# Optimization experiments

Measured on AMD Instinct MI355X. Metric: run time of the kernel, lower is better.

Reference implementation:

```python
import jax, jax.numpy as jnp
import numpy as np

B, N, C1, C2, H = 4, 4096, 320, 256, 5
HD = C1 // H  # 64


def setup_inputs() -> dict:
    key = jax.random.key(0)
    ks = jax.random.split(key, 9)
    w = lambda k, shape, fan_in: jax.random.normal(k, shape, jnp.float32) * (fan_in ** -0.5)
    return {
        "x1": jax.random.normal(ks[0], (B, N, C1), jnp.float32),
        "x2": jax.random.normal(ks[1], (B, N, C2), jnp.float32),
        # nn.Linear weights, torch layout [out_features, in_features]
        "q1_w": w(ks[2], (C1, C1), C1),
        "q2_w": w(ks[3], (C1, C2), C2),
        "kv1_w": w(ks[4], (2 * C1, C2), C2),
        "kv2_w": w(ks[5], (2 * C1, C1), C1),
        "proj1_w": w(ks[6], (C1, C1), C1),
        "proj1_b": jnp.zeros((C1,), jnp.float32),
        "proj2_w": w(ks[7], (C1, C1), C1),
        "proj2_b": jnp.zeros((C1,), jnp.float32),
    }


def _branch(xq, xkv, q_w, kv_w, proj_w, proj_b):
    b, n, _ = xq.shape
    scale = HD ** -0.5
    q = (xq @ q_w.T).reshape(b, n, H, HD).transpose(0, 2, 1, 3)          # [B,H,N,HD]
    kv = (xkv @ kv_w.T).reshape(b, n, 2, H, HD).transpose(2, 0, 3, 1, 4)  # [2,B,H,N,HD]
    k, v = kv[0], kv[1]
    attn = jax.nn.softmax(jnp.einsum('bhqd,bhkd->bhqk', q * scale, k), axis=-1)
    y = jnp.einsum('bhqk,bhkd->bhqd', attn, v)                            # [B,H,N,HD]
    y = y.transpose(0, 2, 1, 3).reshape(b, n, C1)
    return y @ proj_w.T + proj_b


def reference(x1, x2, q1_w, q2_w, kv1_w, kv2_w, proj1_w, proj1_b, proj2_w, proj2_b):
    y1 = _branch(x1, x2, q1_w, kv1_w, proj1_w, proj1_b)  # x1 queries, x2 keys/values
    y2 = _branch(x2, x1, q2_w, kv2_w, proj2_w, proj2_b)  # x2 queries, x1 keys/values
    return jnp.concatenate((y1, y2), axis=-1)            # [B,N,2*C1]
```

## Files before the change

kernel.cpp:

```cpp
#include <hip/hip_runtime.h>
#include <hip/hip_bf16.h>

#define Bb 4
#define Nn 4096
#define C1 320
#define C2 256
#define Hh 5
#define HD 64
#define Mm (Bb*Nn)

using bf16 = __hip_bfloat16;
typedef __attribute__((ext_vector_type(8))) short  short8;
typedef __attribute__((ext_vector_type(4))) short  short4_;
typedef __attribute__((ext_vector_type(4))) float  f32x4;

__device__ __forceinline__ short f2s(float f) {
    bf16 h = __float2bfloat16(f);
    short s;
    __builtin_memcpy(&s, &h, 2);
    return s;
}

__device__ __forceinline__ float fexp2(float x) {
#if __has_builtin(__builtin_amdgcn_exp2f)
    return __builtin_amdgcn_exp2f(x);
#else
    return exp2f(x);
#endif
}

__device__ __forceinline__ int swz(int row, int bb) {
    return row * 64 + ((bb ^ (row & 7)) << 3);
}

struct CvtArgs {
    const float* s[8];
    bf16* d[8];
    int off[9];
};

__global__ void cvt_all(CvtArgs a) {
    int i = (blockIdx.x * blockDim.x + threadIdx.x) * 4;
    if (i >= a.off[8]) return;
    int seg = 0;
    #pragma unroll
    for (int k = 1; k < 8; ++k) seg += (i >= a.off[k]);
    int j = i - a.off[seg];
    float4 v = *(const float4*)(a.s[seg] + j);
    short4_ o = { f2s(v.x), f2s(v.y), f2s(v.z), f2s(v.w) };
    *(short4_*)(a.d[seg] + j) = o;
}

__global__ __launch_bounds__(256) void gemm_proj(
    const bf16* __restrict__ A, const bf16* __restrict__ Wq,
    const bf16* __restrict__ Wkv, int K, float qs,
    bf16* __restrict__ Qo, bf16* __restrict__ Ko, bf16* __restrict__ Vo)
{
    __shared__ bf16 la[128 * 64];
    __shared__ bf16 lw[64 * 64];
    const int m0 = blockIdx.x * 128;
    const bool isq = blockIdx.y < 5;
    const bf16* W = isq ? Wq : Wkv;
    const int n0 = (isq ? blockIdx.y : blockIdx.y - 5) * 64;
    const int t = threadIdx.x;
    const int wave = t >> 6, lane = t & 63, l16 = lane & 15, quad = lane >> 4;
    const int sr = t >> 3, sb = t & 7;

    f32x4 acc[2][4];
    #pragma unroll
    for (int mf = 0; mf < 2; ++mf)
        #pragma unroll
        for (int nt = 0; nt < 4; ++nt) acc[mf][nt] = {0.f,0.f,0.f,0.f};

    const int nk = K >> 6;
    const bf16* ap = A + (size_t)(m0 + sr) * K + sb * 8;
    const bf16* wp = W + (size_t)(n0 + sr) * K + sb * 8;
    short8 ra0 = *(const short8*)ap;
    short8 ra1 = *(const short8*)(ap + (size_t)32 * K);
    short8 ra2 = *(const short8*)(ap + (size_t)64 * K);
    short8 ra3 = *(const short8*)(ap + (size_t)96 * K);
    short8 rw0 = *(const short8*)wp;
    short8 rw1 = *(const short8*)(wp + (size_t)32 * K);

    for (int kt = 0; kt < nk; ++kt) {
        __syncthreads();
        *(short8*)&la[swz(sr,      sb)] = ra0;
        *(short8*)&la[swz(sr + 32, sb)] = ra1;
        *(short8*)&la[swz(sr + 64, sb)] = ra2;
        *(short8*)&la[swz(sr + 96, sb)] = ra3;
        *(short8*)&lw[swz(sr,      sb)] = rw0;
        *(short8*)&lw[swz(sr + 32, sb)] = rw1;
        __syncthreads();
        if (kt + 1 < nk) {
            ap += 64; wp += 64;
            ra0 = *(const short8*)ap;
            ra1 = *(const short8*)(ap + (size_t)32 * K);
            ra2 = *(const short8*)(ap + (size_t)64 * K);
            ra3 = *(const short8*)(ap + (size_t)96 * K);
            rw0 = *(const short8*)wp;
            rw1 = *(const short8*)(wp + (size_t)32 * K);
        }
        const int arow = wave * 32 + l16;
        short8 a00 = *(const short8*)&la[swz(arow,      quad)];
        short8 a01 = *(const short8*)&la[swz(arow,      quad + 4)];
        short8 a10 = *(const short8*)&la[swz(arow + 16, quad)];
        short8 a11 = *(const short8*)&la[swz(arow + 16, quad + 4)];
        #pragma unroll
        for (int nt = 0; nt < 4; ++nt) {
            const int brow = nt * 16 + l16;
            short8 b0 = *(const short8*)&lw[swz(brow, quad)];
            short8 b1 = *(const short8*)&lw[swz(brow, quad + 4)];
            acc[0][nt] = __builtin_amdgcn_mfma_f32_16x16x32_bf16(a00, b0, acc[0][nt], 0, 0, 0);
            acc[0][nt] = __builtin_amdgcn_mfma_f32_16x16x32_bf16(a01, b1, acc[0][nt], 0, 0, 0);
            acc[1][nt] = __builtin_amdgcn_mfma_f32_16x16x32_bf16(a10, b0, acc[1][nt], 0, 0, 0);
            acc[1][nt] = __builtin_amdgcn_mfma_f32_16x16x32_bf16(a11, b1, acc[1][nt], 0, 0, 0);
        }
    }

    const bool isv = !isq && n0 >= C1;
    #pragma unroll
    for (int mf = 0; mf < 2; ++mf) {
        const int mrow = m0 + wave * 32 + mf * 16 + quad * 4;
        if (isq) {
            #pragma unroll
            for (int nt = 0; nt < 4; ++nt) {
                int col = n0 + nt * 16 + l16;
                #pragma unroll
                for (int r = 0; r < 4; ++r)
                    Qo[(size_t)(mrow + r) * C1 + col] = __float2bfloat16(acc[mf][nt][r] * qs);
            }
        } else if (!isv) {
            #pragma unroll
            for (int nt = 0; nt < 4; ++nt) {
                int col = n0 + nt * 16 + l16;
                #pragma unroll
                for (int r = 0; r < 4; ++r)
                    Ko[(size_t)(mrow + r) * C1 + col] = __float2bfloat16(acc[mf][nt][r]);
            }
        } else {
            #pragma unroll
            for (int nt = 0; nt < 4; ++nt) {
                int col = n0 + nt * 16 + l16 - C1;
                int h = col >> 6, d = col & 63;
                #pragma unroll
                for (int r = 0; r < 4; ++r) {
                    int m = mrow + r;
                    int b = m >> 12, n = m & (Nn - 1);
                    Vo[((size_t)(b * Hh + h) * 64 + d) * Nn + n] = __float2bfloat16(acc[mf][nt][r]);
                }
            }
        }
    }
}

__global__ __launch_bounds__(256) void gemm_out(
    const bf16* __restrict__ Y1, const bf16* __restrict__ Wp1, const float* __restrict__ B1,
    const bf16* __restrict__ Y2, const bf16* __restrict__ Wp2, const float* __restrict__ B2,
    float* __restrict__ Of)
{
    __shared__ bf16 la[128 * 64];
    __shared__ bf16 lw[64 * 64];
    const int zz = blockIdx.z;
    const bf16* A = zz ? Y2 : Y1;
    const bf16* W = zz ? Wp2 : Wp1;
    const float* bias = zz ? B2 : B1;
    const int ooff = zz ? C1 : 0;
    const int m0 = blockIdx.x * 128, n0 = blockIdx.y * 64;
    const int t = threadIdx.x;
    const int wave = t >> 6, lane = t & 63, l16 = lane & 15, quad = lane >> 4;
    const int sr = t >> 3, sb = t & 7;
    const int K = C1;

    f32x4 acc[2][4];
    #pragma unroll
    for (int mf = 0; mf < 2; ++mf)
        #pragma unroll
        for (int nt = 0; nt < 4; ++nt) acc[mf][nt] = {0.f,0.f,0.f,0.f};

    const int nk = K >> 6;
    const bf16* ap = A + (size_t)(m0 + sr) * K + sb * 8;
    const bf16* wp = W + (size_t)(n0 + sr) * K + sb * 8;
    short8 ra0 = *(const short8*)ap;
    short8 ra1 = *(const short8*)(ap + (size_t)32 * K);
    short8 ra2 = *(const short8*)(ap + (size_t)64 * K);
    short8 ra3 = *(const short8*)(ap + (size_t)96 * K);
    short8 rw0 = *(const short8*)wp;
    short8 rw1 = *(const short8*)(wp + (size_t)32 * K);

    for (int kt = 0; kt < nk; ++kt) {
        __syncthreads();
        *(short8*)&la[swz(sr,      sb)] = ra0;
        *(short8*)&la[swz(sr + 32, sb)] = ra1;
        *(short8*)&la[swz(sr + 64, sb)] = ra2;
        *(short8*)&la[swz(sr + 96, sb)] = ra3;
        *(short8*)&lw[swz(sr,      sb)] = rw0;
        *(short8*)&lw[swz(sr + 32, sb)] = rw1;
        __syncthreads();
        if (kt + 1 < nk) {
            ap += 64; wp += 64;
            ra0 = *(const short8*)ap;
            ra1 = *(const short8*)(ap + (size_t)32 * K);
            ra2 = *(const short8*)(ap + (size_t)64 * K);
            ra3 = *(const short8*)(ap + (size_t)96 * K);
            rw0 = *(const short8*)wp;
            rw1 = *(const short8*)(wp + (size_t)32 * K);
        }
        const int arow = wave * 32 + l16;
        short8 a00 = *(const short8*)&la[swz(arow,      quad)];
        short8 a01 = *(const short8*)&la[swz(arow,      quad + 4)];
        short8 a10 = *(const short8*)&la[swz(arow + 16, quad)];
        short8 a11 = *(const short8*)&la[swz(arow + 16, quad + 4)];
        #pragma unroll
        for (int nt = 0; nt < 4; ++nt) {
            const int brow = nt * 16 + l16;
            short8 b0 = *(const short8*)&lw[swz(brow, quad)];
            short8 b1 = *(const short8*)&lw[swz(brow, quad + 4)];
            acc[0][nt] = __builtin_amdgcn_mfma_f32_16x16x32_bf16(a00, b0, acc[0][nt], 0, 0, 0);
            acc[0][nt] = __builtin_amdgcn_mfma_f32_16x16x32_bf16(a01, b1, acc[0][nt], 0, 0, 0);
            acc[1][nt] = __builtin_amdgcn_mfma_f32_16x16x32_bf16(a10, b0, acc[1][nt], 0, 0, 0);
            acc[1][nt] = __builtin_amdgcn_mfma_f32_16x16x32_bf16(a11, b1, acc[1][nt], 0, 0, 0);
        }
    }

    #pragma unroll
    for (int mf = 0; mf < 2; ++mf) {
        const int mrow = m0 + wave * 32 + mf * 16 + quad * 4;
        #pragma unroll
        for (int nt = 0; nt < 4; ++nt) {
            int col = n0 + nt * 16 + l16;
            float bv = bias[col];
            #pragma unroll
            for (int r = 0; r < 4; ++r)
                Of[(size_t)(mrow + r) * 640 + ooff + col] = acc[mf][nt][r] + bv;
        }
    }
}

__device__ __forceinline__ unsigned cvtpk(float lo, float hi) {
    unsigned r;
    asm("v_cvt_pk_bf16_f32 %0, %1, %2" : "=v"(r) : "v"(lo), "v"(hi));
    return r;
}

__device__ __forceinline__ void plswap(unsigned &a, unsigned &b) {
#if __has_builtin(__builtin_amdgcn_permlane32_swap)
    auto r = __builtin_amdgcn_permlane32_swap(a, b, false, false);
    a = r[0]; b = r[1];
#else
    asm("v_permlane32_swap_b32 %0, %1" : "+v"(a), "+v"(b));
#endif
}

__device__ __forceinline__ short8 mk8(unsigned d0, unsigned d1, unsigned d2, unsigned d3) {
    union { unsigned u[4]; short8 s; } u;
    u.u[0] = d0; u.u[1] = d1; u.u[2] = d2; u.u[3] = d3;
    return u.s;
}

typedef __attribute__((ext_vector_type(16))) float f32x16;

__global__ __launch_bounds__(256, 2) void flash_kernel(
    const bf16* __restrict__ Q1, const bf16* __restrict__ K1,
    const bf16* __restrict__ V1, bf16* __restrict__ Y1,
    const bf16* __restrict__ Q2, const bf16* __restrict__ K2,
    const bf16* __restrict__ V2, bf16* __restrict__ Y2)
{
    __shared__ bf16 lk[64 * 64];
    __shared__ bf16 lv[64 * 64];
    const int qt = blockIdx.x, h = blockIdx.y, z = blockIdx.z;
    const int b = z & 3, branch = z >> 2;
    const bf16* Q  = branch ? Q2 : Q1;
    const bf16* Km = branch ? K2 : K1;
    const bf16* Vt = branch ? V2 : V1;
    bf16*       Yo = branch ? Y2 : Y1;

    const int t = threadIdx.x;
    const int wave = t >> 6, lane = t & 63;
    const int l32 = lane & 31, hi = lane >> 5;
    const int sr = t >> 3, sb = t & 7;

    const int qrow0 = qt * 256 + wave * 64;

    short8 qf[2][4];
    #pragma unroll
    for (int qb = 0; qb < 2; ++qb) {
        const bf16* qptr = Q + (size_t)(b * Nn + qrow0 + qb * 32 + l32) * C1 + h * HD + hi * 8;
        #pragma unroll
        for (int ksd = 0; ksd < 4; ++ksd)
            qf[qb][ksd] = *(const short8*)(qptr + ksd * 16);
    }

    f32x16 o[2][2];
    #pragma unroll
    for (int qb = 0; qb < 2; ++qb)
        #pragma unroll
        for (int db = 0; db < 2; ++db)
            o[qb][db] = (f32x16){0.f,0.f,0.f,0.f,0.f,0.f,0.f,0.f,0.f,0.f,0.f,0.f,0.f,0.f,0.f,0.f};
    float lsum[2] = {0.f, 0.f};

    const bf16* Kbase = Km + (size_t)b * Nn * C1 + h * HD;
    const bf16* Vbase = Vt + (size_t)(b * Hh + h) * 64 * Nn;

    short8 rk0 = *(const short8*)(Kbase + (size_t)sr * C1 + sb * 8);
    short8 rk1 = *(const short8*)(Kbase + (size_t)(sr + 32) * C1 + sb * 8);
    short8 rv0 = *(const short8*)(Vbase + (size_t)sr * Nn + sb * 8);
    short8 rv1 = *(const short8*)(Vbase + (size_t)(sr + 32) * Nn + sb * 8);

    const int NT = Nn / 64;
    for (int kt = 0; kt < NT; ++kt) {
        __syncthreads();
        *(short8*)&lk[swz(sr, sb)]      = rk0;
        *(short8*)&lk[swz(sr + 32, sb)] = rk1;
        *(short8*)&lv[swz(sr, sb)]      = rv0;
        *(short8*)&lv[swz(sr + 32, sb)] = rv1;
        __syncthreads();
        if (kt + 1 < NT) {
            const int kn = (kt + 1) * 64;
            rk0 = *(const short8*)(Kbase + (size_t)(kn + sr) * C1 + sb * 8);
            rk1 = *(const short8*)(Kbase + (size_t)(kn + sr + 32) * C1 + sb * 8);
            rv0 = *(const short8*)(Vbase + (size_t)sr * Nn + kn + sb * 8);
            rv1 = *(const short8*)(Vbase + (size_t)(sr + 32) * Nn + kn + sb * 8);
        }

        #pragma unroll
        for (int kb = 0; kb < 2; ++kb) {
            short8 ka[4];
            #pragma unroll
            for (int ksd = 0; ksd < 4; ++ksd)
                ka[ksd] = *(const short8*)&lk[swz(kb * 32 + l32, ksd * 2 + hi)];

            short8 pa[2][2];
            #pragma unroll
            for (int qb = 0; qb < 2; ++qb) {
                f32x16 s = (f32x16){0.f,0.f,0.f,0.f,0.f,0.f,0.f,0.f,0.f,0.f,0.f,0.f,0.f,0.f,0.f,0.f};
                #pragma unroll
                for (int ksd = 0; ksd < 4; ++ksd)
                    s = __builtin_amdgcn_mfma_f32_32x32x16_bf16(ka[ksd], qf[qb][ksd], s, 0, 0, 0);
                float p[16];
                #pragma unroll
                for (int r = 0; r < 16; ++r) p[r] = fexp2(s[r]);
                lsum[qb] += (((p[0]+p[1])+(p[2]+p[3])) + ((p[4]+p[5])+(p[6]+p[7])))
                          + (((p[8]+p[9])+(p[10]+p[11])) + ((p[12]+p[13])+(p[14]+p[15])));
                unsigned d0 = cvtpk(p[0],  p[1]),  d2 = cvtpk(p[4],  p[5]);
                plswap(d0, d2);
                unsigned d1 = cvtpk(p[2],  p[3]),  d3 = cvtpk(p[6],  p[7]);
                plswap(d1, d3);
                pa[qb][0] = mk8(d0, d1, d2, d3);
                unsigned e0 = cvtpk(p[8],  p[9]),  e2 = cvtpk(p[12], p[13]);
                plswap(e0, e2);
                unsigned e1 = cvtpk(p[10], p[11]), e3 = cvtpk(p[14], p[15]);
                plswap(e1, e3);
                pa[qb][1] = mk8(e0, e1, e2, e3);
            }

            #pragma unroll
            for (int ks = 0; ks < 2; ++ks) {
                #pragma unroll
                for (int db = 0; db < 2; ++db) {
                    short8 bv = *(const short8*)&lv[swz(db * 32 + l32, kb * 4 + ks * 2 + hi)];
                    o[0][db] = __builtin_amdgcn_mfma_f32_32x32x16_bf16(pa[0][ks], bv, o[0][db], 0, 0, 0);
                    o[1][db] = __builtin_amdgcn_mfma_f32_32x32x16_bf16(pa[1][ks], bv, o[1][db], 0, 0, 0);
                }
            }
        }
    }

    #pragma unroll
    for (int qb = 0; qb < 2; ++qb) {
        float l = lsum[qb] + __shfl_xor(lsum[qb], 32, 64);
        float inv = 1.0f / l;
        #pragma unroll
        for (int r = 0; r < 16; ++r) {
            const int qr = (r & 3) + 8 * (r >> 2) + 4 * hi;
            float invr = __shfl(inv, qr, 64);
            size_t row = (size_t)(b * Nn + qrow0 + qb * 32 + qr);
            #pragma unroll
            for (int db = 0; db < 2; ++db)
                Yo[row * C1 + h * HD + db * 32 + l32] = __float2bfloat16(o[qb][db][r] * invr);
        }
    }
}

extern "C" void kernel_launch(void* const* d_in, const int* in_sizes, int n_in,
                              void* d_out, int out_size, void* d_ws, size_t ws_size,
                              hipStream_t stream)
{
    const float* x1   = (const float*)d_in[0];
    const float* x2   = (const float*)d_in[1];
    const float* q1w  = (const float*)d_in[2];
    const float* q2w  = (const float*)d_in[3];
    const float* kv1w = (const float*)d_in[4];
    const float* kv2w = (const float*)d_in[5];
    const float* p1w  = (const float*)d_in[6];
    const float* p1b  = (const float*)d_in[7];
    const float* p2w  = (const float*)d_in[8];
    const float* p2b  = (const float*)d_in[9];
    float* out = (float*)d_out;

    bf16* ws = (bf16*)d_ws;
    size_t o = 0;
    bf16* x1b  = ws + o; o += (size_t)Mm * C1;
    bf16* x2b  = ws + o; o += (size_t)Mm * C2;
    bf16* wq1  = ws + o; o += C1 * C1;
    bf16* wq2  = ws + o; o += C1 * C2;
    bf16* wkv1 = ws + o; o += 2 * C1 * C2;
    bf16* wkv2 = ws + o; o += 2 * C1 * C1;
    bf16* wp1  = ws + o; o += C1 * C1;
    bf16* wp2  = ws + o; o += C1 * C1;
    bf16* Q1   = ws + o; o += (size_t)Mm * C1;
    bf16* K1   = ws + o; o += (size_t)Mm * C1;
    bf16* V1t  = ws + o; o += (size_t)Mm * C1;
    bf16* Q2   = ws + o; o += (size_t)Mm * C1;
    bf16* K2   = ws + o; o += (size_t)Mm * C1;
    bf16* V2t  = ws + o; o += (size_t)Mm * C1;
    bf16* Y1   = ws + o; o += (size_t)Mm * C1;
    bf16* Y2   = ws + o; o += (size_t)Mm * C1;
    (void)ws_size; (void)in_sizes; (void)n_in; (void)out_size;

    CvtArgs ca;
    ca.s[0] = x1;   ca.d[0] = x1b;  int n0 = Mm * C1;
    ca.s[1] = x2;   ca.d[1] = x2b;  int n1 = Mm * C2;
    ca.s[2] = q1w;  ca.d[2] = wq1;  int n2 = C1 * C1;
    ca.s[3] = q2w;  ca.d[3] = wq2;  int n3 = C1 * C2;
    ca.s[4] = kv1w; ca.d[4] = wkv1; int n4 = 2 * C1 * C2;
    ca.s[5] = kv2w; ca.d[5] = wkv2; int n5 = 2 * C1 * C1;
    ca.s[6] = p1w;  ca.d[6] = wp1;  int n6 = C1 * C1;
    ca.s[7] = p2w;  ca.d[7] = wp2;  int n7 = C1 * C1;
    int ns[8] = {n0, n1, n2, n3, n4, n5, n6, n7};
    ca.off[0] = 0;
    for (int i = 0; i < 8; ++i) ca.off[i + 1] = ca.off[i] + ns[i];
    int total = ca.off[8];
    cvt_all<<<dim3((total / 4 + 255) / 256), 256, 0, stream>>>(ca);

    const float QS = 0.125f * 1.4426950408889634f;

    gemm_proj<<<dim3(Mm / 128, 15), 256, 0, stream>>>(x1b, wq1, wkv2, C1, QS, Q1, K2, V2t);
    gemm_proj<<<dim3(Mm / 128, 15), 256, 0, stream>>>(x2b, wq2, wkv1, C2, QS, Q2, K1, V1t);

    flash_kernel<<<dim3(Nn / 256, Hh, 2 * Bb), 256, 0, stream>>>(Q1, K1, V1t, Y1, Q2, K2, V2t, Y2);

    gemm_out<<<dim3(Mm / 128, C1 / 64, 2), 256, 0, stream>>>(Y1, wp1, p1b, Y2, wp2, p2b, out);
}
```

Measured before the change: 351.0 us.

## Merge projection GEMMs into one launch and halve flash attention block size

The two QKV projection GEMM launches become a single launch with a doubled grid. Each block picks its input, weights, K dimension and outputs from blockIdx.y. The flash attention kernel now uses 128-thread blocks (2 waves, 128 query rows) instead of 256, with the K/V tile staging loop rewritten so each thread loads four rows. This doubles the flash grid to spread work over more CUs and removes one launch, at the cost of each K/V tile being reused by fewer query rows, which doubles K/V global and LDS traffic per query.

Measured after the change: 348.2 us. About the same (-0.8%).

```diff
diff --git a/kernel.cpp b/kernel.cpp
--- a/kernel.cpp
+++ b/kernel.cpp
@@ -13,6 +13,7 @@
 typedef __attribute__((ext_vector_type(8))) short  short8;
 typedef __attribute__((ext_vector_type(4))) short  short4_;
 typedef __attribute__((ext_vector_type(4))) float  f32x4;
+typedef __attribute__((ext_vector_type(16))) float f32x16;
 
 __device__ __forceinline__ short f2s(float f) {
     bf16 h = __float2bfloat16(f);
@@ -33,6 +34,27 @@
     return row * 64 + ((bb ^ (row & 7)) << 3);
 }
 
+__device__ __forceinline__ unsigned cvtpk(float lo, float hi) {
+    unsigned r;
+    asm("v_cvt_pk_bf16_f32 %0, %1, %2" : "=v"(r) : "v"(lo), "v"(hi));
+    return r;
+}
+
+__device__ __forceinline__ void plswap(unsigned &a, unsigned &b) {
+#if __has_builtin(__builtin_amdgcn_permlane32_swap)
+    auto r = __builtin_amdgcn_permlane32_swap(a, b, false, false);
+    a = r[0]; b = r[1];
+#else
+    asm("v_permlane32_swap_b32 %0, %1" : "+v"(a), "+v"(b));
+#endif
+}
+
+__device__ __forceinline__ short8 mk8(unsigned d0, unsigned d1, unsigned d2, unsigned d3) {
+    union { unsigned u[4]; short8 s; } u;
+    u.u[0] = d0; u.u[1] = d1; u.u[2] = d2; u.u[3] = d3;
+    return u.s;
+}
+
 struct CvtArgs {
     const float* s[8];
     bf16* d[8];
@@ -52,16 +74,26 @@
 }
 
 __global__ __launch_bounds__(256) void gemm_proj(
-    const bf16* __restrict__ A, const bf16* __restrict__ Wq,
-    const bf16* __restrict__ Wkv, int K, float qs,
-    bf16* __restrict__ Qo, bf16* __restrict__ Ko, bf16* __restrict__ Vo)
+    const bf16* __restrict__ A1, const bf16* __restrict__ Wq1, const bf16* __restrict__ Wkv1,
+    const bf16* __restrict__ A2, const bf16* __restrict__ Wq2, const bf16* __restrict__ Wkv2,
+    float qs,
+    bf16* __restrict__ Qo1, bf16* __restrict__ Ko1, bf16* __restrict__ Vo1,
+    bf16* __restrict__ Qo2, bf16* __restrict__ Ko2, bf16* __restrict__ Vo2)
 {
     __shared__ bf16 la[128 * 64];
     __shared__ bf16 lw[64 * 64];
     const int m0 = blockIdx.x * 128;
-    const bool isq = blockIdx.y < 5;
-    const bf16* W = isq ? Wq : Wkv;
-    const int n0 = (isq ? blockIdx.y : blockIdx.y - 5) * 64;
+    const int by = blockIdx.y;
+    const int g = (by >= 15);
+    const int yy = by - 15 * g;
+    const int K = g ? C2 : C1;
+    const bf16* A = g ? A2 : A1;
+    const bool isq = yy < 5;
+    const bf16* W = isq ? (g ? Wq2 : Wq1) : (g ? Wkv2 : Wkv1);
+    bf16* Qo = g ? Qo2 : Qo1;
+    bf16* Ko = g ? Ko2 : Ko1;
+    bf16* Vo = g ? Vo2 : Vo1;
+    const int n0 = (isq ? yy : yy - 5) * 64;
     const int t = threadIdx.x;
     const int wave = t >> 6, lane = t & 63, l16 = lane & 15, quad = lane >> 4;
     const int sr = t >> 3, sb = t & 7;
@@ -236,30 +268,7 @@
     }
 }
 
-__device__ __forceinline__ unsigned cvtpk(float lo, float hi) {
-    unsigned r;
-    asm("v_cvt_pk_bf16_f32 %0, %1, %2" : "=v"(r) : "v"(lo), "v"(hi));
-    return r;
-}
-
-__device__ __forceinline__ void plswap(unsigned &a, unsigned &b) {
-#if __has_builtin(__builtin_amdgcn_permlane32_swap)
-    auto r = __builtin_amdgcn_permlane32_swap(a, b, false, false);
-    a = r[0]; b = r[1];
-#else
-    asm("v_permlane32_swap_b32 %0, %1" : "+v"(a), "+v"(b));
-#endif
-}
-
-__device__ __forceinline__ short8 mk8(unsigned d0, unsigned d1, unsigned d2, unsigned d3) {
-    union { unsigned u[4]; short8 s; } u;
-    u.u[0] = d0; u.u[1] = d1; u.u[2] = d2; u.u[3] = d3;
-    return u.s;
-}
-
-typedef __attribute__((ext_vector_type(16))) float f32x16;
-
-__global__ __launch_bounds__(256, 2) void flash_kernel(
+__global__ __launch_bounds__(128, 2) void flash_kernel(
     const bf16* __restrict__ Q1, const bf16* __restrict__ K1,
     const bf16* __restrict__ V1, bf16* __restrict__ Y1,
     const bf16* __restrict__ Q2, const bf16* __restrict__ K2,
@@ -279,7 +288,7 @@
     const int l32 = lane & 31, hi = lane >> 5;
     const int sr = t >> 3, sb = t & 7;
 
-    const int qrow0 = qt * 256 + wave * 64;
+    const int qrow0 = qt * 128 + wave * 64;
 
     short8 qf[2][4];
     #pragma unroll
@@ -301,25 +310,33 @@
     const bf16* Kbase = Km + (size_t)b * Nn * C1 + h * HD;
     const bf16* Vbase = Vt + (size_t)(b * Hh + h) * 64 * Nn;
 
-    short8 rk0 = *(const short8*)(Kbase + (size_t)sr * C1 + sb * 8);
-    short8 rk1 = *(const short8*)(Kbase + (size_t)(sr + 32) * C1 + sb * 8);
-    short8 rv0 = *(const short8*)(Vbase + (size_t)sr * Nn + sb * 8);
-    short8 rv1 = *(const short8*)(Vbase + (size_t)(sr + 32) * Nn + sb * 8);
+    const bf16* kp[4];
+    const bf16* vp[4];
+    short8 rk[4], rv[4];
+    #pragma unroll
+    for (int i = 0; i < 4; ++i) {
+        kp[i] = Kbase + (size_t)(sr + 16 * i) * C1 + sb * 8;
+        vp[i] = Vbase + (size_t)(sr + 16 * i) * Nn + sb * 8;
+        rk[i] = *(const short8*)kp[i];
+        rv[i] = *(const short8*)vp[i];
+    }
 
     const int NT = Nn / 64;
     for (int kt = 0; kt < NT; ++kt) {
         __syncthreads();
-        *(short8*)&lk[swz(sr, sb)]      = rk0;
-        *(short8*)&lk[swz(sr + 32, sb)] = rk1;
-        *(short8*)&lv[swz(sr, sb)]      = rv0;
-        *(short8*)&lv[swz(sr + 32, sb)] = rv1;
+        #pragma unroll
+        for (int i = 0; i < 4; ++i) {
+            *(short8*)&lk[swz(sr + 16 * i, sb)] = rk[i];
+            *(short8*)&lv[swz(sr + 16 * i, sb)] = rv[i];
+        }
         __syncthreads();
         if (kt + 1 < NT) {
-            const int kn = (kt + 1) * 64;
-            rk0 = *(const short8*)(Kbase + (size_t)(kn + sr) * C1 + sb * 8);
-            rk1 = *(const short8*)(Kbase + (size_t)(kn + sr + 32) * C1 + sb * 8);
-            rv0 = *(const short8*)(Vbase + (size_t)sr * Nn + kn + sb * 8);
-            rv1 = *(const short8*)(Vbase + (size_t)(sr + 32) * Nn + kn + sb * 8);
+            #pragma unroll
+            for (int i = 0; i < 4; ++i) {
+                kp[i] += 64 * C1; vp[i] += 64;
+                rk[i] = *(const short8*)kp[i];
+                rv[i] = *(const short8*)vp[i];
+            }
         }
 
         #pragma unroll
@@ -434,10 +451,11 @@
 
     const float QS = 0.125f * 1.4426950408889634f;
 
-    gemm_proj<<<dim3(Mm / 128, 15), 256, 0, stream>>>(x1b, wq1, wkv2, C1, QS, Q1, K2, V2t);
-    gemm_proj<<<dim3(Mm / 128, 15), 256, 0, stream>>>(x2b, wq2, wkv1, C2, QS, Q2, K1, V1t);
-
-    flash_kernel<<<dim3(Nn / 256, Hh, 2 * Bb), 256, 0, stream>>>(Q1, K1, V1t, Y1, Q2, K2, V2t, Y2);
+    gemm_proj<<<dim3(Mm / 128, 30), 256, 0, stream>>>(
+        x1b, wq1, wkv2, x2b, wq2, wkv1, QS,
+        Q1, K2, V2t, Q2, K1, V1t);
+
+    flash_kernel<<<dim3(Nn / 128, Hh, 2 * Bb), 128, 0, stream>>>(Q1, K1, V1t, Y1, Q2, K2, V2t, Y2);
 
     gemm_out<<<dim3(Mm / 128, C1 / 64, 2), 256, 0, stream>>>(Y1, wp1, p1b, Y2, wp2, p2b, out);
 }
```

## Merge projection GEMM launches and shrink flash query tile for more occupancy

Applied to the files above, without the earlier changes.

Fuses the two QKV projection GEMM launches into one grid with 30 column blocks, selecting inputs and weights per block from blockIdx.y. This saves a launch and lets both halves fill the GPU together. The flash attention kernel drops from 64 to 32 query rows per wave (128 per block), doubling the grid and raising launch bounds to 4 blocks per CU. The aim is more waves to hide latency, at the cost of loading K/V tiles twice as often per query row, which halves K/V reuse.

Result: slower. 364.6 us (+3.9%).

```diff
diff --git a/kernel.cpp b/kernel.cpp
--- a/kernel.cpp
+++ b/kernel.cpp
@@ -13,6 +13,7 @@
 typedef __attribute__((ext_vector_type(8))) short  short8;
 typedef __attribute__((ext_vector_type(4))) short  short4_;
 typedef __attribute__((ext_vector_type(4))) float  f32x4;
+typedef __attribute__((ext_vector_type(16))) float f32x16;
 
 __device__ __forceinline__ short f2s(float f) {
     bf16 h = __float2bfloat16(f);
@@ -31,6 +32,27 @@
 
 __device__ __forceinline__ int swz(int row, int bb) {
     return row * 64 + ((bb ^ (row & 7)) << 3);
+}
+
+__device__ __forceinline__ unsigned cvtpk(float lo, float hi) {
+    unsigned r;
+    asm("v_cvt_pk_bf16_f32 %0, %1, %2" : "=v"(r) : "v"(lo), "v"(hi));
+    return r;
+}
+
+__device__ __forceinline__ void plswap(unsigned &a, unsigned &b) {
+#if __has_builtin(__builtin_amdgcn_permlane32_swap)
+    auto r = __builtin_amdgcn_permlane32_swap(a, b, false, false);
+    a = r[0]; b = r[1];
+#else
+    asm("v_permlane32_swap_b32 %0, %1" : "+v"(a), "+v"(b));
+#endif
+}
+
+__device__ __forceinline__ short8 mk8(unsigned d0, unsigned d1, unsigned d2, unsigned d3) {
+    union { unsigned u[4]; short8 s; } u;
+    u.u[0] = d0; u.u[1] = d1; u.u[2] = d2; u.u[3] = d3;
+    return u.s;
 }
 
 struct CvtArgs {
@@ -52,16 +74,26 @@
 }
 
 __global__ __launch_bounds__(256) void gemm_proj(
-    const bf16* __restrict__ A, const bf16* __restrict__ Wq,
-    const bf16* __restrict__ Wkv, int K, float qs,
-    bf16* __restrict__ Qo, bf16* __restrict__ Ko, bf16* __restrict__ Vo)
+    const bf16* __restrict__ A1, const bf16* __restrict__ Wq1, const bf16* __restrict__ Wkv1,
+    const bf16* __restrict__ A2, const bf16* __restrict__ Wq2, const bf16* __restrict__ Wkv2,
+    float qs,
+    bf16* __restrict__ Qo1, bf16* __restrict__ Ko1, bf16* __restrict__ Vo1,
+    bf16* __restrict__ Qo2, bf16* __restrict__ Ko2, bf16* __restrict__ Vo2)
 {
     __shared__ bf16 la[128 * 64];
     __shared__ bf16 lw[64 * 64];
     const int m0 = blockIdx.x * 128;
-    const bool isq = blockIdx.y < 5;
-    const bf16* W = isq ? Wq : Wkv;
-    const int n0 = (isq ? blockIdx.y : blockIdx.y - 5) * 64;
+    const int by = blockIdx.y;
+    const int g = (by >= 15);
+    const int yy = by - 15 * g;
+    const int K = g ? C2 : C1;
+    const bf16* A = g ? A2 : A1;
+    const bool isq = yy < 5;
+    const bf16* W = isq ? (g ? Wq2 : Wq1) : (g ? Wkv2 : Wkv1);
+    bf16* Qo = g ? Qo2 : Qo1;
+    bf16* Ko = g ? Ko2 : Ko1;
+    bf16* Vo = g ? Vo2 : Vo1;
+    const int n0 = (isq ? yy : yy - 5) * 64;
     const int t = threadIdx.x;
     const int wave = t >> 6, lane = t & 63, l16 = lane & 15, quad = lane >> 4;
     const int sr = t >> 3, sb = t & 7;
@@ -236,30 +268,7 @@
     }
 }
 
-__device__ __forceinline__ unsigned cvtpk(float lo, float hi) {
-    unsigned r;
-    asm("v_cvt_pk_bf16_f32 %0, %1, %2" : "=v"(r) : "v"(lo), "v"(hi));
-    return r;
-}
-
-__device__ __forceinline__ void plswap(unsigned &a, unsigned &b) {
-#if __has_builtin(__builtin_amdgcn_permlane32_swap)
-    auto r = __builtin_amdgcn_permlane32_swap(a, b, false, false);
-    a = r[0]; b = r[1];
-#else
-    asm("v_permlane32_swap_b32 %0, %1" : "+v"(a), "+v"(b));
-#endif
-}
-
-__device__ __forceinline__ short8 mk8(unsigned d0, unsigned d1, unsigned d2, unsigned d3) {
-    union { unsigned u[4]; short8 s; } u;
-    u.u[0] = d0; u.u[1] = d1; u.u[2] = d2; u.u[3] = d3;
-    return u.s;
-}
-
-typedef __attribute__((ext_vector_type(16))) float f32x16;
-
-__global__ __launch_bounds__(256, 2) void flash_kernel(
+__global__ __launch_bounds__(256, 4) void flash_kernel(
     const bf16* __restrict__ Q1, const bf16* __restrict__ K1,
     const bf16* __restrict__ V1, bf16* __restrict__ Y1,
     const bf16* __restrict__ Q2, const bf16* __restrict__ K2,
@@ -279,24 +288,20 @@
     const int l32 = lane & 31, hi = lane >> 5;
     const int sr = t >> 3, sb = t & 7;
 
-    const int qrow0 = qt * 256 + wave * 64;
-
-    short8 qf[2][4];
-    #pragma unroll
-    for (int qb = 0; qb < 2; ++qb) {
-        const bf16* qptr = Q + (size_t)(b * Nn + qrow0 + qb * 32 + l32) * C1 + h * HD + hi * 8;
+    const int qrow0 = qt * 128 + wave * 32;
+
+    short8 qf[4];
+    {
+        const bf16* qptr = Q + (size_t)(b * Nn + qrow0 + l32) * C1 + h * HD + hi * 8;
         #pragma unroll
         for (int ksd = 0; ksd < 4; ++ksd)
-            qf[qb][ksd] = *(const short8*)(qptr + ksd * 16);
-    }
-
-    f32x16 o[2][2];
-    #pragma unroll
-    for (int qb = 0; qb < 2; ++qb)
-        #pragma unroll
-        for (int db = 0; db < 2; ++db)
-            o[qb][db] = (f32x16){0.f,0.f,0.f,0.f,0.f,0.f,0.f,0.f,0.f,0.f,0.f,0.f,0.f,0.f,0.f,0.f};
-    float lsum[2] = {0.f, 0.f};
+            qf[ksd] = *(const short8*)(qptr + ksd * 16);
+    }
+
+    f32x16 o[2];
+    o[0] = (f32x16){0.f,0.f,0.f,0.f,0.f,0.f,0.f,0.f,0.f,0.f,0.f,0.f,0.f,0.f,0.f,0.f};
+    o[1] = o[0];
+    float lsum = 0.f;
 
     const bf16* Kbase = Km + (size_t)b * Nn * C1 + h * HD;
     const bf16* Vbase = Vt + (size_t)(b * Hh + h) * 64 * Nn;
@@ -329,28 +334,29 @@
             for (int ksd = 0; ksd < 4; ++ksd)
                 ka[ksd] = *(const short8*)&lk[swz(kb * 32 + l32, ksd * 2 + hi)];
 
-            short8 pa[2][2];
-            #pragma unroll
-            for (int qb = 0; qb < 2; ++qb) {
-                f32x16 s = (f32x16){0.f,0.f,0.f,0.f,0.f,0.f,0.f,0.f,0.f,0.f,0.f,0.f,0.f,0.f,0.f,0.f};
-                #pragma unroll
-                for (int ksd = 0; ksd < 4; ++ksd)
-                    s = __builtin_amdgcn_mfma_f32_32x32x16_bf16(ka[ksd], qf[qb][ksd], s, 0, 0, 0);
-                float p[16];
-                #pragma unroll
-                for (int r = 0; r < 16; ++r) p[r] = fexp2(s[r]);
-                lsum[qb] += (((p[0]+p[1])+(p[2]+p[3])) + ((p[4]+p[5])+(p[6]+p[7])))
-                          + (((p[8]+p[9])+(p[10]+p[11])) + ((p[12]+p[13])+(p[14]+p[15])));
+            f32x16 s = (f32x16){0.f,0.f,0.f,0.f,0.f,0.f,0.f,0.f,0.f,0.f,0.f,0.f,0.f,0.f,0.f,0.f};
+            #pragma unroll
+            for (int ksd = 0; ksd < 4; ++ksd)
+                s = __builtin_amdgcn_mfma_f32_32x32x16_bf16(ka[ksd], qf[ksd], s, 0, 0, 0);
+
+            float p[16];
+            #pragma unroll
+            for (int r = 0; r < 16; ++r) p[r] = fexp2(s[r]);
+            lsum += (((p[0]+p[1])+(p[2]+p[3])) + ((p[4]+p[5])+(p[6]+p[7])))
+                  + (((p[8]+p[9])+(p[10]+p[11])) + ((p[12]+p[13])+(p[14]+p[15])));
+
+            short8 pa[2];
+            {
                 unsigned d0 = cvtpk(p[0],  p[1]),  d2 = cvtpk(p[4],  p[5]);
                 plswap(d0, d2);
                 unsigned d1 = cvtpk(p[2],  p[3]),  d3 = cvtpk(p[6],  p[7]);
                 plswap(d1, d3);
-                pa[qb][0] = mk8(d0, d1, d2, d3);
+                pa[0] = mk8(d0, d1, d2, d3);
                 unsigned e0 = cvtpk(p[8],  p[9]),  e2 = cvtpk(p[12], p[13]);
                 plswap(e0, e2);
                 unsigned e1 = cvtpk(p[10], p[11]), e3 = cvtpk(p[14], p[15]);
                 plswap(e1, e3);
-                pa[qb][1] = mk8(e0, e1, e2, e3);
+                pa[1] = mk8(e0, e1, e2, e3);
             }
 
             #pragma unroll
@@ -358,25 +364,23 @@
                 #pragma unroll
                 for (int db = 0; db < 2; ++db) {
                     short8 bv = *(const short8*)&lv[swz(db * 32 + l32, kb * 4 + ks * 2 + hi)];
-                    o[0][db] = __builtin_amdgcn_mfma_f32_32x32x16_bf16(pa[0][ks], bv, o[0][db], 0, 0, 0);
-                    o[1][db] = __builtin_amdgcn_mfma_f32_32x32x16_bf16(pa[1][ks], bv, o[1][db], 0, 0, 0);
+                    o[db] = __builtin_amdgcn_mfma_f32_32x32x16_bf16(pa[ks], bv, o[db], 0, 0, 0);
                 }
             }
         }
     }
 
-    #pragma unroll
-    for (int qb = 0; qb < 2; ++qb) {
-        float l = lsum[qb] + __shfl_xor(lsum[qb], 32, 64);
+    {
+        float l = lsum + __shfl_xor(lsum, 32, 64);
         float inv = 1.0f / l;
         #pragma unroll
         for (int r = 0; r < 16; ++r) {
             const int qr = (r & 3) + 8 * (r >> 2) + 4 * hi;
             float invr = __shfl(inv, qr, 64);
-            size_t row = (size_t)(b * Nn + qrow0 + qb * 32 + qr);
+            size_t row = (size_t)(b * Nn + qrow0 + qr);
             #pragma unroll
             for (int db = 0; db < 2; ++db)
-                Yo[row * C1 + h * HD + db * 32 + l32] = __float2bfloat16(o[qb][db][r] * invr);
+                Yo[row * C1 + h * HD + db * 32 + l32] = __float2bfloat16(o[db][r] * invr);
         }
     }
 }
@@ -434,10 +438,11 @@
 
     const float QS = 0.125f * 1.4426950408889634f;
 
-    gemm_proj<<<dim3(Mm / 128, 15), 256, 0, stream>>>(x1b, wq1, wkv2, C1, QS, Q1, K2, V2t);
-    gemm_proj<<<dim3(Mm / 128, 15), 256, 0, stream>>>(x2b, wq2, wkv1, C2, QS, Q2, K1, V1t);
-
-    flash_kernel<<<dim3(Nn / 256, Hh, 2 * Bb), 256, 0, stream>>>(Q1, K1, V1t, Y1, Q2, K2, V2t, Y2);
+    gemm_proj<<<dim3(Mm / 128, 30), 256, 0, stream>>>(
+        x1b, wq1, wkv2, x2b, wq2, wkv1, QS,
+        Q1, K2, V2t, Q2, K1, V1t);
+
+    flash_kernel<<<dim3(Nn / 128, Hh, 2 * Bb), 256, 0, stream>>>(Q1, K1, V1t, Y1, Q2, K2, V2t, Y2);
 
     gemm_out<<<dim3(Mm / 128, C1 / 64, 2), 256, 0, stream>>>(Y1, wp1, p1b, Y2, wp2, p2b, out);
 }
```
